# Kernel optimization log

Measured on AMD Instinct MI355X. Metric: run time of the kernel, lower is better.

Reference implementation:

```python
import jax, jax.numpy as jnp
import numpy as np

TAU = 0.05
BETA = 8.0
MAX_ITERS = 6
EPS = 1e-12  # torch F.normalize eps


def setup_inputs() -> dict:
    key = jax.random.key(0)
    P, d, C, h = 20000, 128, 512, 4
    k1, k2, k3, k4 = jax.random.split(key, 4)
    K = jax.random.normal(k1, (P, d), dtype=jnp.float32) * 0.1
    Theta = jax.random.normal(k2, (C, d, h), dtype=jnp.float32)
    head_idx = jax.random.randint(k3, (C,), 0, P)
    initial_val = jax.random.uniform(k4, (P,), dtype=jnp.float32)
    return {"K": K, "Theta": Theta, "head_idx": head_idx, "initial_val": initial_val}


def _l2norm(x, axis):
    n = jnp.sqrt(jnp.sum(x * x, axis=axis, keepdims=True))
    return x / jnp.maximum(n, EPS)


def reference(K, Theta, head_idx, initial_val):
    P = K.shape[0]
    C, d, h = Theta.shape
    Kn = _l2norm(K, axis=1)            # [P, d]
    Thetan = _l2norm(Theta, axis=1)    # [C, d, h] (normalize over d, per slot)
    # cosine similarity per clause/slot: S[c, p, s]
    S = jnp.einsum('pd,cds->cps', Kn, Thetan)          # [C, P, h]
    best = jnp.argmax(S, axis=1)                        # [C, h] best predicate per slot
    conf = jnp.take_along_axis(S, best[:, None, :], axis=1)[:, 0, :]  # [C, h]
    beta_eff = max(BETA, 1.0)
    n = 2 * h
    log_n = jnp.float32(np.log(n))

    val = initial_val
    for _ in range(MAX_ITERS):
        vals = val[best]                                # [C, h] truth values at argmax preds
        combined = jnp.concatenate([conf, vals], axis=1)  # [C, 2h]
        # softmin_tau(x) = -(1/tau) * (logsumexp(-x/tau) - log n)
        g = -(1.0 / TAU) * (jax.nn.logsumexp(-combined / TAU, axis=1) - log_n)
        g = jnp.clip(g, 0.0, 1.0)                       # [C]
        # soft OR per head: (1/beta) * logsumexp(beta * g) over clauses sharing a head
        e = jax.ops.segment_sum(jnp.exp(beta_eff * g), head_idx, num_segments=P)
        g_head = jnp.log(jnp.maximum(e, 1e-38)) / beta_eff
        val = jnp.where(e > 0, jnp.maximum(val, g_head), val)
    return val
```

## Files before the change

kernel.cpp:

```cpp
#include <hip/hip_runtime.h>
#include <hip/hip_bf16.h>
#include <math.h>

#define D_DIM 128
#define H_DIM 4

typedef __attribute__((ext_vector_type(4))) float f32x4;
typedef __attribute__((ext_vector_type(8))) __bf16 bf16x8v;

__device__ inline unsigned short f2bf(float f) {
    __hip_bfloat16 b = __float2bfloat16(f);
    return *reinterpret_cast<unsigned short*>(&b);
}

__global__ __launch_bounds__(256) void k_prep(
    const float* __restrict__ K, unsigned int* __restrict__ Knb,
    float* __restrict__ rnK,
    const float* __restrict__ Theta, unsigned int* __restrict__ Tnb,
    float* __restrict__ Tn32,
    const float* __restrict__ initial, float* __restrict__ out,
    int* __restrict__ head_of, int P, int Ppad, int NJ)
{
    int wave = threadIdx.x >> 6, lane = threadIdx.x & 63;

    int row = blockIdx.x * 4 + wave;
    if (row < Ppad) {
        if (row >= P) {
            Knb[(size_t)row * 64 + lane] = 0u;
        } else {
            float2 v = ((const float2*)(K + (size_t)row * D_DIM))[lane];
            float ss = v.x * v.x + v.y * v.y;
            #pragma unroll
            for (int off = 1; off < 64; off <<= 1) ss += __shfl_xor(ss, off);
            float rn = 1.0f / fmaxf(sqrtf(ss), 1e-12f);
            unsigned int pk = (unsigned)f2bf(v.x * rn) | ((unsigned)f2bf(v.y * rn) << 16);
            Knb[(size_t)row * 64 + lane] = pk;
            if (lane == 0) {
                rnK[row] = rn;
                out[row] = initial[row];
                head_of[row] = 0x7FFFFFFF;
            }
        }
    }

    if (blockIdx.x < (NJ >> 2)) {
        int j = blockIdx.x * 4 + wave;
        int c = j >> 2, s = j & 3;
        const float* base = Theta + (size_t)c * (D_DIM * H_DIM) + s;
        float t0 = base[(2 * lane) * H_DIM];
        float t1 = base[(2 * lane + 1) * H_DIM];
        float ss = t0 * t0 + t1 * t1;
        #pragma unroll
        for (int off = 1; off < 64; off <<= 1) ss += __shfl_xor(ss, off);
        float rn = 1.0f / fmaxf(sqrtf(ss), 1e-12f);
        float n0 = t0 * rn, n1 = t1 * rn;
        Tnb[(size_t)j * 64 + lane] = (unsigned)f2bf(n0) | ((unsigned)f2bf(n1) << 16);
        float2 w; w.x = n0; w.y = n1;
        ((float2*)(Tn32 + (size_t)j * D_DIM))[lane] = w;
    }
}

__global__ __launch_bounds__(256) void k_mfma_max(
    const unsigned short* __restrict__ Knb, const unsigned short* __restrict__ Tnb,
    float* __restrict__ pv2, const int* __restrict__ head_idx,
    int* __restrict__ head_of, int C, int NT4, int NBLK)
{
    __shared__ __align__(16) unsigned short As[128 * 128];
    __shared__ __align__(16) unsigned short Bs[128 * 128];

    int tid = threadIdx.x;
    int orig = blockIdx.x;
    if (orig == 0) {
        for (int g = tid; g < C; g += 256) atomicMin(&head_of[head_idx[g]], g);
    }
    int q = NBLK >> 3, r = NBLK & 7;
    int xcd = orig & 7, idx = orig >> 3;
    int wgid = (xcd < r ? xcd * (q + 1) : r * (q + 1) + (xcd - r) * q) + idx;
    int pt = wgid >> 4, jt = wgid & 15;
    int p0 = pt * 128, j0 = jt * 128;
    int lane = tid & 63;
    int wave = tid >> 6;

    {
        int rr = lane >> 4, cc = lane & 15;
        const unsigned short* gA = Tnb + (size_t)j0 * 128;
        const unsigned short* gB = Knb + (size_t)p0 * 128;
        #pragma unroll
        for (int i = 0; i < 8; i++) {
            int r0 = wave * 32 + i * 4;
            int rw = r0 + rr;
            int sc = (cc ^ (rw & 7)) << 3;
            __builtin_amdgcn_global_load_lds(
                (const __attribute__((address_space(1))) unsigned int*)(gA + (size_t)rw * 128 + sc),
                (__attribute__((address_space(3))) unsigned int*)&As[r0 * 128], 16, 0, 0);
            __builtin_amdgcn_global_load_lds(
                (const __attribute__((address_space(1))) unsigned int*)(gB + (size_t)rw * 128 + sc),
                (__attribute__((address_space(3))) unsigned int*)&Bs[r0 * 128], 16, 0, 0);
        }
    }
    __syncthreads();

    int wm = wave >> 1, wn = wave & 1;
    int lr = lane & 15, lg = lane >> 4;

    f32x4 acc[4][4];
    #pragma unroll
    for (int m = 0; m < 4; m++)
        #pragma unroll
        for (int n = 0; n < 4; n++) { f32x4 z = {0.f, 0.f, 0.f, 0.f}; acc[m][n] = z; }

    #pragma unroll
    for (int ks = 0; ks < 4; ks++) {
        int koff = (8 * lg + 32 * ks) ^ ((lr & 7) << 3);
        bf16x8v af[4], bv[4];
        #pragma unroll
        for (int m = 0; m < 4; m++) {
            int row = 64 * wm + 16 * m + lr;
            af[m] = *(const bf16x8v*)&As[row * 128 + koff];
        }
        #pragma unroll
        for (int n = 0; n < 4; n++) {
            int row = 64 * wn + 16 * n + lr;
            bv[n] = *(const bf16x8v*)&Bs[row * 128 + koff];
        }
        #pragma unroll
        for (int m = 0; m < 4; m++)
            #pragma unroll
            for (int n = 0; n < 4; n++)
                acc[m][n] = __builtin_amdgcn_mfma_f32_16x16x32_bf16(af[m], bv[n], acc[m][n], 0, 0, 0);
    }

    __syncthreads();
    float* red = (float*)As;
    #pragma unroll
    for (int m = 0; m < 4; m++) {
        #pragma unroll
        for (int n2 = 0; n2 < 2; n2++) {
            f32x4 a0 = acc[m][2 * n2], a1 = acc[m][2 * n2 + 1];
            float t0 = fmaxf(a0[0], a1[0]);
            float t1 = fmaxf(a0[1], a1[1]);
            float t2 = fmaxf(a0[2], a1[2]);
            float t3 = fmaxf(a0[3], a1[3]);
            #pragma unroll
            for (int off = 1; off <= 8; off <<= 1) {
                t0 = fmaxf(t0, __shfl_xor(t0, off));
                t1 = fmaxf(t1, __shfl_xor(t1, off));
                t2 = fmaxf(t2, __shfl_xor(t2, off));
                t3 = fmaxf(t3, __shfl_xor(t3, off));
            }
            if (lr == 0) {
                int jb = 64 * wm + 16 * m + 4 * lg;
                int ch = 2 * wn + n2;
                red[(jb + 0) * 4 + ch] = t0;
                red[(jb + 1) * 4 + ch] = t1;
                red[(jb + 2) * 4 + ch] = t2;
                red[(jb + 3) * 4 + ch] = t3;
            }
        }
    }
    __syncthreads();
    #pragma unroll
    for (int e = tid; e < 512; e += 256) {
        int jl = e >> 2, ch = e & 3;
        pv2[(size_t)(j0 + jl) * NT4 + pt * 4 + ch] = red[jl * 4 + ch];
    }
}

__global__ __launch_bounds__(256) void k_prune(
    const float* __restrict__ pv2, const float* __restrict__ K,
    const float* __restrict__ rnK, const float* __restrict__ Tn32,
    float* __restrict__ conf, int* __restrict__ best, int P, int NT4)
{
    int wave = threadIdx.x >> 6, lane = threadIdx.x & 63;
    int j = blockIdx.x * 4 + wave;
    const float* row = pv2 + (size_t)j * NT4;

    float v[10];
    float m = -INFINITY;
    #pragma unroll
    for (int i = 0; i < 10; i++) {
        int t = lane + i * 64;
        v[i] = (t < NT4) ? row[t] : -INFINITY;
        m = fmaxf(m, v[i]);
    }
    #pragma unroll
    for (int off = 32; off; off >>= 1) m = fmaxf(m, __shfl_xor(m, off));
    float thr = m - 0.009f;

    float bv = -INFINITY; int bbp = 0x7FFFFFFF;
    int half = lane & 1;
    int pl = lane >> 1;
    #pragma unroll
    for (int i = 0; i < 10; i++) {
        unsigned long long ball = __ballot(v[i] >= thr);
        while (ball) {
            int bit = __ffsll(ball) - 1;
            ball &= ball - 1;
            int t = i * 64 + bit;
            int p = t * 32 + pl;
            bool ok = (p < P);
            int pc = ok ? p : 0;
            const float4* kp = (const float4*)(K + (size_t)pc * D_DIM + half * 64);
            const float4* tp = (const float4*)(Tn32 + (size_t)j * D_DIM + half * 64);
            float sx = 0.f, sy = 0.f, sz = 0.f, sw = 0.f;
            #pragma unroll
            for (int k4 = 0; k4 < 16; k4++) {
                float4 a = kp[k4], b = tp[k4];
                sx = fmaf(a.x, b.x, sx); sy = fmaf(a.y, b.y, sy);
                sz = fmaf(a.z, b.z, sz); sw = fmaf(a.w, b.w, sw);
            }
            float dot = (sx + sy) + (sz + sw);
            dot += __shfl_xor(dot, 1);
            float vv = ok ? dot * rnK[pc] : -INFINITY;
            int bp = p;
            #pragma unroll
            for (int off = 2; off < 64; off <<= 1) {
                float ov = __shfl_xor(vv, off);
                int op = __shfl_xor(bp, off);
                if (ov > vv || (ov == vv && op < bp)) { vv = ov; bp = op; }
            }
            if (vv > bv || (vv == bv && bp < bbp)) { bv = vv; bbp = bp; }
        }
    }
    if (lane == 0) { conf[j] = bv; best[j] = bbp; }
}

__global__ __launch_bounds__(1024) void k_logic(
    const int* __restrict__ head_idx, const float* __restrict__ initial_val,
    const float* __restrict__ conf, const int* __restrict__ best,
    const int* __restrict__ head_of,
    float* __restrict__ out, int C)
{
    __shared__ float hval[1024];
    __shared__ float elds[1024];
    int c = threadIdx.x;
    int h = head_idx[c];
    int myslot = head_of[h];
    hval[c] = initial_val[h];

    float cf[H_DIM], v0[H_DIM]; int bs[H_DIM];
    #pragma unroll
    for (int s = 0; s < H_DIM; s++) {
        int b = best[c * H_DIM + s];
        cf[s] = conf[c * H_DIM + s];
        v0[s] = initial_val[b];
        int ho = head_of[b];
        bs[s] = (ho < C) ? ho : -1;
    }
    __syncthreads();

    const float inv_tau = 20.0f;
    const float logn = logf(2.0f * H_DIM);
    const float beta = 8.0f;

    for (int it = 0; it < 6; it++) {
        float x[2 * H_DIM];
        #pragma unroll
        for (int s = 0; s < H_DIM; s++) {
            x[s] = cf[s];
            x[H_DIM + s] = (bs[s] >= 0) ? hval[bs[s]] : v0[s];
        }
        float cur = hval[myslot];
        elds[c] = 0.f;
        __syncthreads();

        float m = x[0];
        #pragma unroll
        for (int i = 1; i < 2 * H_DIM; i++) m = fminf(m, x[i]);
        float ssum = 0.f;
        #pragma unroll
        for (int i = 0; i < 2 * H_DIM; i++) ssum += expf((m - x[i]) * inv_tau);
        float g = -inv_tau * ((-m * inv_tau + logf(ssum)) - logn);
        g = fminf(fmaxf(g, 0.f), 1.f);
        float w = expf(beta * g);
        atomicAdd(&elds[myslot], w);
        __syncthreads();

        float e = elds[myslot];
        float gh = logf(fmaxf(e, 1e-38f)) / beta;
        float nv = fmaxf(cur, gh);
        if (myslot == c) hval[c] = nv;
        __syncthreads();
    }

    if (myslot == c) out[h] = hval[c];
}

extern "C" void kernel_launch(void* const* d_in, const int* in_sizes, int n_in,
                              void* d_out, int out_size, void* d_ws, size_t ws_size,
                              hipStream_t stream) {
    const float* K        = (const float*)d_in[0];
    const float* Theta    = (const float*)d_in[1];
    const int*   head_idx = (const int*)d_in[2];
    const float* initial  = (const float*)d_in[3];
    float* out = (float*)d_out;

    int P  = in_sizes[3];
    int C  = in_sizes[2];
    int NJ = C * H_DIM;
    int Ppad = ((P + 127) / 128) * 128;
    int NT = Ppad / 128;
    int NT4 = NT * 4;
    int NBLK = NT * (NJ / 128);

    char* w = (char*)d_ws;
    size_t off = 0;
    auto alloc = [&](size_t bytes) { void* p = w + off; off += (bytes + 255) & ~(size_t)255; return p; };
    unsigned int* Knb  = (unsigned int*)alloc((size_t)Ppad * D_DIM * 2);
    unsigned int* Tnb  = (unsigned int*)alloc((size_t)NJ * D_DIM * 2);
    float* Tn32 = (float*)alloc((size_t)NJ * D_DIM * 4);
    float* rnK  = (float*)alloc((size_t)P * 4);
    float* pv2  = (float*)alloc((size_t)NJ * NT4 * 4);
    float* conf = (float*)alloc((size_t)NJ * 4);
    int*   best = (int*)alloc((size_t)NJ * 4);
    int* head_of = (int*)alloc((size_t)P * 4);
    (void)ws_size;

    k_prep<<<Ppad / 4, 256, 0, stream>>>(K, Knb, rnK, Theta, Tnb, Tn32,
                                         initial, out, head_of, P, Ppad, NJ);

    k_mfma_max<<<NBLK, 256, 0, stream>>>((const unsigned short*)Knb,
                                         (const unsigned short*)Tnb, pv2,
                                         head_idx, head_of, C, NT4, NBLK);

    k_prune<<<NJ / 4, 256, 0, stream>>>(pv2, K, rnK, Tn32, conf, best, P, NT4);
    k_logic<<<1, C, 0, stream>>>(head_idx, initial, conf, best, head_of, out, C);
}
```

Before: 77.18 us.

## Fuse all stages into one cooperative persistent kernel with grid syncs

Replaces the four kernel launches with a single cooperative kernel of 256 blocks of 512 threads that runs prep, the MFMA tile max, pruning and the logic iterations, separated by grid-wide syncs. The goal is to remove per-launch overhead and the gaps between launches. The MFMA phase becomes a persistent loop over tiles ordered so consecutive tiles share a P-tile, which lets it skip reloading the K operand into LDS. In exchange the grid is fixed in size, each block carries grid-sync cost, and the final logic stage runs on a single block while the others idle. If the cooperative launch fails, the code falls back to the original four kernels.

```diff
diff --git a/kernel.cpp b/kernel.cpp
--- a/kernel.cpp
+++ b/kernel.cpp
@@ -1,6 +1,9 @@
 #include <hip/hip_runtime.h>
 #include <hip/hip_bf16.h>
+#include <hip/hip_cooperative_groups.h>
 #include <math.h>
+
+namespace cg = cooperative_groups;
 
 #define D_DIM 128
 #define H_DIM 4
@@ -11,6 +14,267 @@
 __device__ inline unsigned short f2bf(float f) {
     __hip_bfloat16 b = __float2bfloat16(f);
     return *reinterpret_cast<unsigned short*>(&b);
+}
+
+__global__ __launch_bounds__(512, 2) void k_mega(
+    const float* __restrict__ K, const float* __restrict__ Theta,
+    const int* __restrict__ head_idx, const float* __restrict__ initial,
+    float* __restrict__ out,
+    unsigned int* __restrict__ Knb, unsigned int* __restrict__ Tnb,
+    float* __restrict__ Tn32, float* __restrict__ rnK,
+    float* __restrict__ pv2, float* __restrict__ conf, int* __restrict__ best,
+    int* __restrict__ head_of,
+    int P, int Ppad, int NT4, int C, int NJ)
+{
+    cg::grid_group gg = cg::this_grid();
+    __shared__ __align__(16) unsigned short As[128 * 128];
+    __shared__ __align__(16) unsigned short Bs[128 * 128];
+
+    const int tid  = threadIdx.x;
+    const int lane = tid & 63;
+    const int wave = tid >> 6;
+    const int nb   = gridDim.x;
+    const int b    = blockIdx.x;
+    const int gw   = b * 8 + wave;
+
+    for (int i = b * 512 + tid; i < P; i += nb * 512) {
+        out[i] = initial[i];
+        head_of[i] = 0x7FFFFFFF;
+    }
+    for (int row = gw; row < Ppad; row += nb * 8) {
+        if (row >= P) {
+            Knb[(size_t)row * 64 + lane] = 0u;
+        } else {
+            float2 v = ((const float2*)(K + (size_t)row * D_DIM))[lane];
+            float ss = v.x * v.x + v.y * v.y;
+            #pragma unroll
+            for (int off = 1; off < 64; off <<= 1) ss += __shfl_xor(ss, off);
+            float rn = 1.0f / fmaxf(sqrtf(ss), 1e-12f);
+            Knb[(size_t)row * 64 + lane] =
+                (unsigned)f2bf(v.x * rn) | ((unsigned)f2bf(v.y * rn) << 16);
+            if (lane == 0) rnK[row] = rn;
+        }
+    }
+    for (int j = gw; j < NJ; j += nb * 8) {
+        int c = j >> 2, s = j & 3;
+        const float* base = Theta + (size_t)c * (D_DIM * H_DIM) + s;
+        float t0 = base[(2 * lane) * H_DIM];
+        float t1 = base[(2 * lane + 1) * H_DIM];
+        float ss = t0 * t0 + t1 * t1;
+        #pragma unroll
+        for (int off = 1; off < 64; off <<= 1) ss += __shfl_xor(ss, off);
+        float rn = 1.0f / fmaxf(sqrtf(ss), 1e-12f);
+        float n0 = t0 * rn, n1 = t1 * rn;
+        Tnb[(size_t)j * 64 + lane] = (unsigned)f2bf(n0) | ((unsigned)f2bf(n1) << 16);
+        float2 w; w.x = n0; w.y = n1;
+        ((float2*)(Tn32 + (size_t)j * D_DIM))[lane] = w;
+    }
+    gg.sync();
+
+    if (b == 0) {
+        for (int g = tid; g < C; g += 512) atomicMin(&head_of[head_idx[g]], g);
+    }
+    const int xcd = b & 7, idx = b >> 3;
+    const int lb = xcd * (nb >> 3) + idx;
+    const int total = (Ppad >> 7) * 16;
+    const int q = total / nb, r = total % nb;
+    const int begin = (lb < r) ? lb * (q + 1) : r * (q + 1) + (lb - r) * q;
+    const int cnt   = (lb < r) ? q + 1 : q;
+    const unsigned short* KnbS = (const unsigned short*)Knb;
+    const unsigned short* TnbS = (const unsigned short*)Tnb;
+    const int wm = wave >> 2, wn = wave & 3;
+    const int lr = lane & 15, lg = lane >> 4;
+    int cur_pt = -1;
+
+    for (int itt = 0; itt < cnt; ++itt) {
+        int wgid = begin + itt;
+        int pt = wgid >> 4, jt = wgid & 15;
+        int p0 = pt * 128, j0 = jt * 128;
+        bool newp = (pt != cur_pt);
+        cur_pt = pt;
+        {
+            int rr = lane >> 4, c15 = lane & 15;
+            const unsigned short* gA = TnbS + (size_t)j0 * 128;
+            const unsigned short* gB = KnbS + (size_t)p0 * 128;
+            #pragma unroll
+            for (int i = 0; i < 4; i++) {
+                int r0 = wave * 16 + i * 4;
+                int rw = r0 + rr;
+                int sc = (c15 ^ (rw & 7)) << 3;
+                __builtin_amdgcn_global_load_lds(
+                    (const __attribute__((address_space(1))) unsigned int*)(gA + (size_t)rw * 128 + sc),
+                    (__attribute__((address_space(3))) unsigned int*)&As[r0 * 128], 16, 0, 0);
+                if (newp)
+                    __builtin_amdgcn_global_load_lds(
+                        (const __attribute__((address_space(1))) unsigned int*)(gB + (size_t)rw * 128 + sc),
+                        (__attribute__((address_space(3))) unsigned int*)&Bs[r0 * 128], 16, 0, 0);
+            }
+        }
+        __syncthreads();
+
+        f32x4 acc[4][2];
+        #pragma unroll
+        for (int m = 0; m < 4; m++)
+            #pragma unroll
+            for (int n = 0; n < 2; n++) { f32x4 z = {0.f, 0.f, 0.f, 0.f}; acc[m][n] = z; }
+
+        #pragma unroll
+        for (int ks = 0; ks < 4; ks++) {
+            int koff = (8 * lg + 32 * ks) ^ ((lr & 7) << 3);
+            bf16x8v af[4], bv[2];
+            #pragma unroll
+            for (int m = 0; m < 4; m++)
+                af[m] = *(const bf16x8v*)&As[(64 * wm + 16 * m + lr) * 128 + koff];
+            #pragma unroll
+            for (int n = 0; n < 2; n++)
+                bv[n] = *(const bf16x8v*)&Bs[(32 * wn + 16 * n + lr) * 128 + koff];
+            #pragma unroll
+            for (int m = 0; m < 4; m++)
+                #pragma unroll
+                for (int n = 0; n < 2; n++)
+                    acc[m][n] = __builtin_amdgcn_mfma_f32_16x16x32_bf16(af[m], bv[n], acc[m][n], 0, 0, 0);
+        }
+        __syncthreads();
+
+        float* red = (float*)As;
+        #pragma unroll
+        for (int m = 0; m < 4; m++) {
+            f32x4 a0 = acc[m][0], a1 = acc[m][1];
+            float t0 = fmaxf(a0[0], a1[0]);
+            float t1 = fmaxf(a0[1], a1[1]);
+            float t2 = fmaxf(a0[2], a1[2]);
+            float t3 = fmaxf(a0[3], a1[3]);
+            #pragma unroll
+            for (int off = 1; off <= 8; off <<= 1) {
+                t0 = fmaxf(t0, __shfl_xor(t0, off));
+                t1 = fmaxf(t1, __shfl_xor(t1, off));
+                t2 = fmaxf(t2, __shfl_xor(t2, off));
+                t3 = fmaxf(t3, __shfl_xor(t3, off));
+            }
+            if (lr == 0) {
+                int jb = 64 * wm + 16 * m + 4 * lg;
+                red[(jb + 0) * 4 + wn] = t0;
+                red[(jb + 1) * 4 + wn] = t1;
+                red[(jb + 2) * 4 + wn] = t2;
+                red[(jb + 3) * 4 + wn] = t3;
+            }
+        }
+        __syncthreads();
+        {
+            int jl = tid >> 2, ch = tid & 3;
+            pv2[(size_t)(j0 + jl) * NT4 + pt * 4 + ch] = red[jl * 4 + ch];
+        }
+        __syncthreads();
+    }
+    gg.sync();
+
+    for (int jj = gw; jj < NJ; jj += nb * 8) {
+        const float* row = pv2 + (size_t)jj * NT4;
+        float v[10];
+        float m = -INFINITY;
+        #pragma unroll
+        for (int i = 0; i < 10; i++) {
+            int t = lane + i * 64;
+            v[i] = (t < NT4) ? row[t] : -INFINITY;
+            m = fmaxf(m, v[i]);
+        }
+        #pragma unroll
+        for (int off = 32; off; off >>= 1) m = fmaxf(m, __shfl_xor(m, off));
+        float thr = m - 0.009f;
+
+        float bv = -INFINITY; int bbp = 0x7FFFFFFF;
+        int half = lane & 1;
+        int pl = lane >> 1;
+        #pragma unroll
+        for (int i = 0; i < 10; i++) {
+            unsigned long long ball = __ballot(v[i] >= thr);
+            while (ball) {
+                int bit = __ffsll(ball) - 1;
+                ball &= ball - 1;
+                int t = i * 64 + bit;
+                int p = t * 32 + pl;
+                bool ok = (p < P);
+                int pc = ok ? p : 0;
+                const float4* kp = (const float4*)(K + (size_t)pc * D_DIM + half * 64);
+                const float4* tp = (const float4*)(Tn32 + (size_t)jj * D_DIM + half * 64);
+                float sx = 0.f, sy = 0.f, sz = 0.f, sw = 0.f;
+                #pragma unroll
+                for (int k4 = 0; k4 < 16; k4++) {
+                    float4 a = kp[k4], bb = tp[k4];
+                    sx = fmaf(a.x, bb.x, sx); sy = fmaf(a.y, bb.y, sy);
+                    sz = fmaf(a.z, bb.z, sz); sw = fmaf(a.w, bb.w, sw);
+                }
+                float dot = (sx + sy) + (sz + sw);
+                dot += __shfl_xor(dot, 1);
+                float vv = ok ? dot * rnK[pc] : -INFINITY;
+                int bp = p;
+                #pragma unroll
+                for (int off = 2; off < 64; off <<= 1) {
+                    float ov = __shfl_xor(vv, off);
+                    int op = __shfl_xor(bp, off);
+                    if (ov > vv || (ov == vv && op < bp)) { vv = ov; bp = op; }
+                }
+                if (vv > bv || (vv == bv && bp < bbp)) { bv = vv; bbp = bp; }
+            }
+        }
+        if (lane == 0) { conf[jj] = bv; best[jj] = bbp; }
+    }
+    gg.sync();
+
+    if (b == 0) {
+        float* hval = (float*)As;
+        float* elds = hval + 512;
+        int c = tid;
+        int h = head_idx[c];
+        int myslot = head_of[h];
+        hval[c] = initial[h];
+
+        float cf[H_DIM], v0[H_DIM]; int bs[H_DIM];
+        #pragma unroll
+        for (int s = 0; s < H_DIM; s++) {
+            int bb = best[c * H_DIM + s];
+            cf[s] = conf[c * H_DIM + s];
+            v0[s] = initial[bb];
+            int ho = head_of[bb];
+            bs[s] = (ho < C) ? ho : -1;
+        }
+        __syncthreads();
+
+        const float inv_tau = 20.0f;
+        const float logn = logf(2.0f * H_DIM);
+        const float beta = 8.0f;
+
+        for (int it = 0; it < 6; it++) {
+            float x[2 * H_DIM];
+            #pragma unroll
+            for (int s = 0; s < H_DIM; s++) {
+                x[s] = cf[s];
+                x[H_DIM + s] = (bs[s] >= 0) ? hval[bs[s]] : v0[s];
+            }
+            float cur = hval[myslot];
+            elds[c] = 0.f;
+            __syncthreads();
+
+            float m = x[0];
+            #pragma unroll
+            for (int i = 1; i < 2 * H_DIM; i++) m = fminf(m, x[i]);
+            float ssum = 0.f;
+            #pragma unroll
+            for (int i = 0; i < 2 * H_DIM; i++) ssum += expf((m - x[i]) * inv_tau);
+            float g = -inv_tau * ((-m * inv_tau + logf(ssum)) - logn);
+            g = fminf(fmaxf(g, 0.f), 1.f);
+            atomicAdd(&elds[myslot], expf(beta * g));
+            __syncthreads();
+
+            float e = elds[myslot];
+            float gh = logf(fmaxf(e, 1e-38f)) / beta;
+            float nv = fmaxf(cur, gh);
+            if (myslot == c) hval[c] = nv;
+            __syncthreads();
+        }
+
+        if (myslot == c) out[h] = hval[c];
+    }
 }
 
 __global__ __launch_bounds__(256) void k_prep(
@@ -22,7 +286,6 @@
     int* __restrict__ head_of, int P, int Ppad, int NJ)
 {
     int wave = threadIdx.x >> 6, lane = threadIdx.x & 63;
-
     int row = blockIdx.x * 4 + wave;
     if (row < Ppad) {
         if (row >= P) {
@@ -33,8 +296,8 @@
             #pragma unroll
             for (int off = 1; off < 64; off <<= 1) ss += __shfl_xor(ss, off);
             float rn = 1.0f / fmaxf(sqrtf(ss), 1e-12f);
-            unsigned int pk = (unsigned)f2bf(v.x * rn) | ((unsigned)f2bf(v.y * rn) << 16);
-            Knb[(size_t)row * 64 + lane] = pk;
+            Knb[(size_t)row * 64 + lane] =
+                (unsigned)f2bf(v.x * rn) | ((unsigned)f2bf(v.y * rn) << 16);
             if (lane == 0) {
                 rnK[row] = rn;
                 out[row] = initial[row];
@@ -42,7 +305,6 @@
             }
         }
     }
-
     if (blockIdx.x < (NJ >> 2)) {
         int j = blockIdx.x * 4 + wave;
         int c = j >> 2, s = j & 3;
@@ -67,7 +329,6 @@
 {
     __shared__ __align__(16) unsigned short As[128 * 128];
     __shared__ __align__(16) unsigned short Bs[128 * 128];
-
     int tid = threadIdx.x;
     int orig = blockIdx.x;
     if (orig == 0) {
@@ -80,16 +341,15 @@
     int p0 = pt * 128, j0 = jt * 128;
     int lane = tid & 63;
     int wave = tid >> 6;
-
     {
-        int rr = lane >> 4, cc = lane & 15;
+        int rr = lane >> 4, ccc = lane & 15;
         const unsigned short* gA = Tnb + (size_t)j0 * 128;
         const unsigned short* gB = Knb + (size_t)p0 * 128;
         #pragma unroll
         for (int i = 0; i < 8; i++) {
             int r0 = wave * 32 + i * 4;
             int rw = r0 + rr;
-            int sc = (cc ^ (rw & 7)) << 3;
+            int sc = (ccc ^ (rw & 7)) << 3;
             __builtin_amdgcn_global_load_lds(
                 (const __attribute__((address_space(1))) unsigned int*)(gA + (size_t)rw * 128 + sc),
                 (__attribute__((address_space(3))) unsigned int*)&As[r0 * 128], 16, 0, 0);
@@ -99,37 +359,29 @@
         }
     }
     __syncthreads();
-
     int wm = wave >> 1, wn = wave & 1;
     int lr = lane & 15, lg = lane >> 4;
-
     f32x4 acc[4][4];
     #pragma unroll
     for (int m = 0; m < 4; m++)
         #pragma unroll
         for (int n = 0; n < 4; n++) { f32x4 z = {0.f, 0.f, 0.f, 0.f}; acc[m][n] = z; }
-
     #pragma unroll
     for (int ks = 0; ks < 4; ks++) {
         int koff = (8 * lg + 32 * ks) ^ ((lr & 7) << 3);
         bf16x8v af[4], bv[4];
         #pragma unroll
-        for (int m = 0; m < 4; m++) {
-            int row = 64 * wm + 16 * m + lr;
-            af[m] = *(const bf16x8v*)&As[row * 128 + koff];
-        }
-        #pragma unroll
-        for (int n = 0; n < 4; n++) {
-            int row = 64 * wn + 16 * n + lr;
-            bv[n] = *(const bf16x8v*)&Bs[row * 128 + koff];
-        }
+        for (int m = 0; m < 4; m++)
+            af[m] = *(const bf16x8v*)&As[(64 * wm + 16 * m + lr) * 128 + koff];
+        #pragma unroll
+        for (int n = 0; n < 4; n++)
+            bv[n] = *(const bf16x8v*)&Bs[(64 * wn + 16 * n + lr) * 128 + koff];
         #pragma unroll
         for (int m = 0; m < 4; m++)
             #pragma unroll
             for (int n = 0; n < 4; n++)
                 acc[m][n] = __builtin_amdgcn_mfma_f32_16x16x32_bf16(af[m], bv[n], acc[m][n], 0, 0, 0);
     }
-
     __syncthreads();
     float* red = (float*)As;
     #pragma unroll
@@ -174,7 +426,6 @@
     int wave = threadIdx.x >> 6, lane = threadIdx.x & 63;
     int j = blockIdx.x * 4 + wave;
     const float* row = pv2 + (size_t)j * NT4;
-
     float v[10];
     float m = -INFINITY;
     #pragma unroll
@@ -186,7 +437,6 @@
     #pragma unroll
     for (int off = 32; off; off >>= 1) m = fmaxf(m, __shfl_xor(m, off));
     float thr = m - 0.009f;
-
     float bv = -INFINITY; int bbp = 0x7FFFFFFF;
     int half = lane & 1;
     int pl = lane >> 1;
@@ -205,9 +455,9 @@
             float sx = 0.f, sy = 0.f, sz = 0.f, sw = 0.f;
             #pragma unroll
             for (int k4 = 0; k4 < 16; k4++) {
-                float4 a = kp[k4], b = tp[k4];
-                sx = fmaf(a.x, b.x, sx); sy = fmaf(a.y, b.y, sy);
-                sz = fmaf(a.z, b.z, sz); sw = fmaf(a.w, b.w, sw);
+                float4 a = kp[k4], bb = tp[k4];
+                sx = fmaf(a.x, bb.x, sx); sy = fmaf(a.y, bb.y, sy);
+                sz = fmaf(a.z, bb.z, sz); sw = fmaf(a.w, bb.w, sw);
             }
             float dot = (sx + sy) + (sz + sw);
             dot += __shfl_xor(dot, 1);
@@ -237,7 +487,6 @@
     int h = head_idx[c];
     int myslot = head_of[h];
     hval[c] = initial_val[h];
-
     float cf[H_DIM], v0[H_DIM]; int bs[H_DIM];
     #pragma unroll
     for (int s = 0; s < H_DIM; s++) {
@@ -248,11 +497,9 @@
         bs[s] = (ho < C) ? ho : -1;
     }
     __syncthreads();
-
     const float inv_tau = 20.0f;
     const float logn = logf(2.0f * H_DIM);
     const float beta = 8.0f;
-
     for (int it = 0; it < 6; it++) {
         float x[2 * H_DIM];
         #pragma unroll
@@ -263,7 +510,6 @@
         float cur = hval[myslot];
         elds[c] = 0.f;
         __syncthreads();
-
         float m = x[0];
         #pragma unroll
         for (int i = 1; i < 2 * H_DIM; i++) m = fminf(m, x[i]);
@@ -272,17 +518,14 @@
         for (int i = 0; i < 2 * H_DIM; i++) ssum += expf((m - x[i]) * inv_tau);
         float g = -inv_tau * ((-m * inv_tau + logf(ssum)) - logn);
         g = fminf(fmaxf(g, 0.f), 1.f);
-        float w = expf(beta * g);
-        atomicAdd(&elds[myslot], w);
-        __syncthreads();
-
+        atomicAdd(&elds[myslot], expf(beta * g));
+        __syncthreads();
         float e = elds[myslot];
         float gh = logf(fmaxf(e, 1e-38f)) / beta;
         float nv = fmaxf(cur, gh);
         if (myslot == c) hval[c] = nv;
         __syncthreads();
     }
-
     if (myslot == c) out[h] = hval[c];
 }
 
@@ -314,15 +557,20 @@
     float* conf = (float*)alloc((size_t)NJ * 4);
     int*   best = (int*)alloc((size_t)NJ * 4);
     int* head_of = (int*)alloc((size_t)P * 4);
-    (void)ws_size;
-
-    k_prep<<<Ppad / 4, 256, 0, stream>>>(K, Knb, rnK, Theta, Tnb, Tn32,
-                                         initial, out, head_of, P, Ppad, NJ);
-
-    k_mfma_max<<<NBLK, 256, 0, stream>>>((const unsigned short*)Knb,
-                                         (const unsigned short*)Tnb, pv2,
-                                         head_idx, head_of, C, NT4, NBLK);
-
-    k_prune<<<NJ / 4, 256, 0, stream>>>(pv2, K, rnK, Tn32, conf, best, P, NT4);
-    k_logic<<<1, C, 0, stream>>>(head_idx, initial, conf, best, head_of, out, C);
-}
+    (void)ws_size; (void)n_in; (void)out_size;
+
+    void* args[] = { &K, &Theta, &head_idx, &initial, &out,
+                     &Knb, &Tnb, &Tn32, &rnK, &pv2, &conf, &best, &head_of,
+                     &P, &Ppad, &NT4, &C, &NJ };
+    hipError_t err = hipLaunchCooperativeKernel((const void*)k_mega, dim3(256), dim3(512),
+                                                args, 0, stream);
+    if (err != hipSuccess) {
+        k_prep<<<Ppad / 4, 256, 0, stream>>>(K, Knb, rnK, Theta, Tnb, Tn32,
+                                             initial, out, head_of, P, Ppad, NJ);
+        k_mfma_max<<<NBLK, 256, 0, stream>>>((const unsigned short*)Knb,
+                                             (const unsigned short*)Tnb, pv2,
+                                             head_idx, head_of, C, NT4, NBLK);
+        k_prune<<<NJ / 4, 256, 0, stream>>>(pv2, K, rnK, Tn32, conf, best, P, NT4);
+        k_logic<<<1, C, 0, stream>>>(head_idx, initial, conf, best, head_of, out, C);
+    }
+}
```

After: 174.9 us. 127% more time.
